# Performance work log

Measured on AMD Instinct MI355X. Metric: run time of the kernel, lower is better.

The kernel has to match this reference:

```python
import jax, jax.numpy as jnp
import numpy as np

NUM_USERS = 100000
NUM_ITEMS = 50000
EMB_DIM = 64
NNZ = 4800000
BATCH = 16384
N_LAYERS = 3


def setup_inputs() -> dict:
    key = jax.random.key(0)
    k0, k1, k2, k3, k4, k5 = jax.random.split(key, 6)
    N = NUM_USERS + NUM_ITEMS
    rows = jax.random.randint(k0, (NNZ,), 0, N, dtype=jnp.int32)
    cols = jax.random.randint(k1, (NNZ,), 0, N, dtype=jnp.int32)
    # symmetric normalization values: 1/sqrt(deg_out * deg_in), as in LightGCN preprocessing
    ones = jnp.ones((NNZ,), jnp.float32)
    deg_r = jax.ops.segment_sum(ones, rows, num_segments=N)
    deg_c = jax.ops.segment_sum(ones, cols, num_segments=N)
    vals = 1.0 / jnp.sqrt(jnp.maximum(deg_r[rows], 1.0) * jnp.maximum(deg_c[cols], 1.0))
    user_emb = 0.1 * jax.random.normal(k2, (NUM_USERS, EMB_DIM), jnp.float32)
    item_emb = 0.1 * jax.random.normal(k3, (NUM_ITEMS, EMB_DIM), jnp.float32)
    user_idx = jax.random.randint(k4, (BATCH,), 0, NUM_USERS, dtype=jnp.int64)
    item_idx = jax.random.randint(k5, (BATCH,), 0, NUM_ITEMS, dtype=jnp.int64)
    return {
        "user_emb": user_emb,
        "item_emb": item_emb,
        "rows": rows,
        "cols": cols,
        "vals": vals,
        "user_idx": user_idx,
        "item_idx": item_idx,
        "n_layers": N_LAYERS,
    }


def reference(user_emb, item_emb, rows, cols, vals, user_idx, item_idx, n_layers):
    num_users = user_emb.shape[0]
    N = num_users + item_emb.shape[0]
    all_emb = jnp.concatenate([user_emb, item_emb], axis=0)  # [N, D]
    acc = all_emb  # running sum over layer embeddings (embs[0] = E)
    emb = all_emb
    for _ in range(n_layers):
        # SpMM: out[r] = sum_{edges (r,c)} vals * emb[c]
        emb = jax.ops.segment_sum(vals[:, None] * emb[cols], rows, num_segments=N)
        acc = acc + emb
    light_out = acc / jnp.float32(n_layers + 1)  # mean over stacked layers
    u_e = light_out[user_idx]                     # [B, D]
    i_e = light_out[num_users + item_idx]         # [B, D]
    return (u_e * i_e).sum(axis=-1)               # [B]
```

## Files before the change

### kernel.cpp

```cpp
#include <hip/hip_runtime.h>
#include <hip/hip_fp16.h>

#define NUM_USERS 100000
#define NUM_ITEMS 50000
#define NN (NUM_USERS + NUM_ITEMS)
#define EMB_DIM 64
#define BATCH 16384
#define RPA 512
#define NBA ((NN + RPA - 1) / RPA)
#define SLOT 22528
#define NBLKA 768
#define CAP 16
#define OVF 32
#define SENT (1 << 27)
#define RSLOT 72

__device__ __forceinline__ unsigned h2u(__half2 h) {
    union { __half2 h; unsigned u; } x; x.h = h; return x.u;
}
__device__ __forceinline__ __half2 u2h(unsigned u) {
    union { __half2 h; unsigned u; } x; x.u = u; return x.h;
}

__global__ void lgcn_prep(unsigned long long* __restrict__ gq,
                          unsigned char* __restrict__ flags) {
    int i = blockIdx.x * blockDim.x + threadIdx.x;
    if (i < NBA) gq[i] = 0;
    for (int j = i; j < NN / 4; j += gridDim.x * blockDim.x)
        ((unsigned*)flags)[j] = 0;
    if (i == 0)
        for (int j = (NN / 4) * 4; j < NN; ++j) flags[j] = 0;
}

__global__ void __launch_bounds__(512) lgcn_binA(
        const float4* __restrict__ user_emb, const float4* __restrict__ item_emb,
        uint2* __restrict__ embh, int n_user4, int n_tot4,
        const int* __restrict__ rows, const int* __restrict__ cols,
        const float* __restrict__ vals, unsigned long long* __restrict__ gq,
        int2* __restrict__ cv_tmp, int nnz, int epb) {
    __shared__ int2 stage[CAP][NBA];
    __shared__ int  hist[NBA];
    __shared__ int  SBase[NBA];
    __shared__ int  pcnt[NBA];
    __shared__ int4 ovfBuf[2][OVF];
    __shared__ int  ovfCnt[2];
    int t = threadIdx.x;

    for (int i = blockIdx.x * 512 + t; i < n_tot4; i += NBLKA * 512) {
        float4 v = (i < n_user4) ? user_emb[i] : item_emb[i - n_user4];
        uint2 o;
        o.x = h2u(__float22half2_rn(make_float2(v.x, v.y)));
        o.y = h2u(__float22half2_rn(make_float2(v.z, v.w)));
        embh[i] = o;
    }

    int base = blockIdx.x * epb;
    int end  = base + epb; if (end > nnz) end = nnz;
    if (t < NBA) { hist[t] = 0; pcnt[t] = 0; }
    if (t == 0) { ovfCnt[0] = 0; ovfCnt[1] = 0; }
    __syncthreads();
    for (int i = base + t; i < end; i += 512)
        atomicAdd(&hist[rows[i] >> 9], 1);
    __syncthreads();
    if (t < NBA) {
        int c = hist[t];
        int p = 0;
        if (c) {
            int cp = (c + 7) & ~7;
            unsigned long long old = atomicAdd(&gq[t],
                ((unsigned long long)c << 32) | (unsigned)cp);
            p = (int)(unsigned)old;
        }
        SBase[t] = p;
    }
    __syncthreads();

    int p = 0;
    for (int r0 = base; r0 < end; r0 += 1024, p ^= 1) {
        int no = ovfCnt[p ^ 1];
        for (int j = t; j < no; j += 512) {
            int4 e = ovfBuf[p ^ 1][j];
            int b = e.w;
            int k = atomicAdd(&pcnt[b], 1);
            if (k < CAP) stage[k][b] = make_int2(e.x, e.y);
            else { int q = atomicAdd(&ovfCnt[p], 1);
                   if (q < OVF) ovfBuf[p][q] = e; }
        }
#pragma unroll
        for (int q2 = 0; q2 < 2; ++q2) {
            int i = r0 + q2 * 512 + t;
            if (i < end) {
                int r = rows[i];
                int b = r >> 9;
                __half hv = __float2half(vals[i]);
                int ex = ((r & 511) << 18) | cols[i];
                int ey = (int)h2u(__half2half2(hv));
                int k = atomicAdd(&pcnt[b], 1);
                if (k < CAP) stage[k][b] = make_int2(ex, ey);
                else { int q = atomicAdd(&ovfCnt[p], 1);
                       if (q < OVF) ovfBuf[p][q] = make_int4(ex, ey, 0, b); }
            }
        }
        __syncthreads();
        if (t < NBA) {
            int c = pcnt[t]; if (c > CAP) c = CAP;
            int g = c & ~7;
            if (g) {
                long long gb = (long long)t * SLOT + SBase[t];
                int4* dst = (int4*)&cv_tmp[gb];
                for (int j = 0; j < g; j += 2) {
                    int2 e0 = stage[j][t];
                    int2 e1 = stage[j + 1][t];
                    dst[j >> 1] = make_int4(e0.x, e0.y, e1.x, e1.y);
                }
                SBase[t] += g;
                for (int j = g; j < c; ++j) stage[j - g][t] = stage[j][t];
            }
            pcnt[t] = c - g;
        }
        if (t == 0) ovfCnt[p ^ 1] = 0;
        __syncthreads();
    }

    {
        int no = ovfCnt[p ^ 1];
        for (int j = t; j < no; j += 512) {
            int4 e = ovfBuf[p ^ 1][j];
            int b = e.w;
            int k = atomicAdd(&pcnt[b], 1);
            if (k < CAP) stage[k][b] = make_int2(e.x, e.y);
            else cv_tmp[(long long)b * SLOT + SBase[b] + k] =
                     make_int2(e.x, e.y);
        }
    }
    __syncthreads();
    if (t < NBA) {
        int c_raw = pcnt[t];
        int cl = min(c_raw, CAP);
        long long gb = (long long)t * SLOT + SBase[t];
        for (int j = 0; j < cl; ++j) cv_tmp[gb + j] = stage[j][t];
        int cp = (c_raw + 7) & ~7;
        for (int j = c_raw; j < cp; ++j) cv_tmp[gb + j] = make_int2(SENT, 0);
    }
}

#define BINB_PUT(p) do { int x = (p).x; if (!(x & SENT)) {                   \
    int rl = (x >> 18) & 511; int pos = atomicAdd(&cnt[rl], 1);              \
    if (pos < RSLOT) { int v16 = (p).y & 0xFFFF;                             \
        cv[(long long)(r0 + rl) * RSLOT + pos] =                             \
            (((v16 + 2) >> 2) << 18) | (x & 0x3FFFF); } } } while (0)

__global__ void __launch_bounds__(1024) lgcn_binB(
        const unsigned long long* __restrict__ gq,
        const int2* __restrict__ cv_tmp, int* __restrict__ cv,
        int* __restrict__ deg,
        const int* __restrict__ user_idx, const int* __restrict__ item_idx,
        unsigned char* __restrict__ flags) {
    __shared__ int cnt[RPA];
    int s = blockIdx.x;
    int t = threadIdx.x;
    long long w0 = (long long)s * SLOT;
    int wlen = (int)(unsigned)gq[s];
    int r0 = s * RPA;
    if (t < RPA) cnt[t] = 0;
    __syncthreads();
    int i = t;
    for (; i + 3 * 1024 < wlen; i += 4096) {
        int2 p0 = cv_tmp[w0 + i];
        int2 p1 = cv_tmp[w0 + i + 1024];
        int2 p2 = cv_tmp[w0 + i + 2048];
        int2 p3 = cv_tmp[w0 + i + 3072];
        BINB_PUT(p0); BINB_PUT(p1); BINB_PUT(p2); BINB_PUT(p3);
    }
    for (; i < wlen; i += 1024) {
        int2 p = cv_tmp[w0 + i];
        BINB_PUT(p);
    }
    for (int j = s * 1024 + t; j < BATCH; j += NBA * 1024) {
        flags[user_idx[j]] = 1;
        flags[NUM_USERS + item_idx[j]] = 1;
    }
    __syncthreads();
    if (t < RPA) {
        int r = r0 + t;
        if (r < NN) deg[r] = min(cnt[t], RSLOT);
    }
}

__global__ void __launch_bounds__(256) lgcn_spmm(
        const int* __restrict__ deg,
        const int* __restrict__ cv,
        const uint4* __restrict__ embh,
        uint4* __restrict__ nxth,
        const unsigned char* __restrict__ flags, int sel,
        const uint4* __restrict__ e0t, const uint4* __restrict__ e1t,
        float4* __restrict__ sums) {
    int wid = (blockIdx.x * blockDim.x + threadIdx.x) >> 6;
    int lane = threadIdx.x & 63;
    if (wid >= NN) return;
    if (sel && !flags[wid]) return;
    int n = deg[wid];
    int grp  = lane >> 3;
    int dim8 = lane & 7;
    const int* ep = cv + (long long)wid * RSLOT;

    __half2 c0 = __float2half2_rn(0.f);
    __half2 c1 = c0, c2 = c0, c3 = c0;
    int m = n >> 3;
    int k = 0;
    for (; k + 4 <= m; k += 4) {
        int p[4]; uint4 raw[4];
#pragma unroll
        for (int j = 0; j < 4; ++j) p[j] = ep[8 * (k + j) + grp];
#pragma unroll
        for (int j = 0; j < 4; ++j)
            raw[j] = embh[(long long)(p[j] & 0x3FFFF) * 8 + dim8];
#pragma unroll
        for (int j = 0; j < 4; ++j) {
            unsigned vv = ((unsigned)p[j] >> 18) << 2;
            __half2 v2 = u2h(vv | (vv << 16));
            c0 = __hfma2(v2, u2h(raw[j].x), c0);
            c1 = __hfma2(v2, u2h(raw[j].y), c1);
            c2 = __hfma2(v2, u2h(raw[j].z), c2);
            c3 = __hfma2(v2, u2h(raw[j].w), c3);
        }
    }
    for (; k + 2 <= m; k += 2) {
        int p[2]; uint4 raw[2];
#pragma unroll
        for (int j = 0; j < 2; ++j) p[j] = ep[8 * (k + j) + grp];
#pragma unroll
        for (int j = 0; j < 2; ++j)
            raw[j] = embh[(long long)(p[j] & 0x3FFFF) * 8 + dim8];
#pragma unroll
        for (int j = 0; j < 2; ++j) {
            unsigned vv = ((unsigned)p[j] >> 18) << 2;
            __half2 v2 = u2h(vv | (vv << 16));
            c0 = __hfma2(v2, u2h(raw[j].x), c0);
            c1 = __hfma2(v2, u2h(raw[j].y), c1);
            c2 = __hfma2(v2, u2h(raw[j].z), c2);
            c3 = __hfma2(v2, u2h(raw[j].w), c3);
        }
    }
    for (; k < m; ++k) {
        int p = ep[8 * k + grp];
        uint4 raw = embh[(long long)(p & 0x3FFFF) * 8 + dim8];
        unsigned vv = ((unsigned)p >> 18) << 2;
        __half2 v2 = u2h(vv | (vv << 16));
        c0 = __hfma2(v2, u2h(raw.x), c0);
        c1 = __hfma2(v2, u2h(raw.y), c1);
        c2 = __hfma2(v2, u2h(raw.z), c2);
        c3 = __hfma2(v2, u2h(raw.w), c3);
    }
    int rem = n & 7;
    if (grp < rem) {
        int p = ep[8 * m + grp];
        uint4 raw = embh[(long long)(p & 0x3FFFF) * 8 + dim8];
        unsigned vv = ((unsigned)p >> 18) << 2;
        __half2 v2 = u2h(vv | (vv << 16));
        c0 = __hfma2(v2, u2h(raw.x), c0);
        c1 = __hfma2(v2, u2h(raw.y), c1);
        c2 = __hfma2(v2, u2h(raw.z), c2);
        c3 = __hfma2(v2, u2h(raw.w), c3);
    }

#pragma unroll
    for (int off = 8; off < 64; off <<= 1) {
        c0 = __hadd2(c0, u2h(__shfl_xor(h2u(c0), off)));
        c1 = __hadd2(c1, u2h(__shfl_xor(h2u(c1), off)));
        c2 = __hadd2(c2, u2h(__shfl_xor(h2u(c2), off)));
        c3 = __hadd2(c3, u2h(__shfl_xor(h2u(c3), off)));
    }
    if (grp == 0) {
        long long o = (long long)wid * 8 + dim8;
        if (!sel) {
            uint4 ov;
            ov.x = h2u(c0); ov.y = h2u(c1); ov.z = h2u(c2); ov.w = h2u(c3);
            nxth[o] = ov;
        } else {
            uint4 r0v = e0t[o], r1v = e1t[o], r2v = embh[o];
            float2 f0 = __half22float2(c0), f1 = __half22float2(c1);
            float2 f2 = __half22float2(c2), f3 = __half22float2(c3);
            float2 a;
            a = __half22float2(u2h(r0v.x)); f0.x += a.x; f0.y += a.y;
            a = __half22float2(u2h(r1v.x)); f0.x += a.x; f0.y += a.y;
            a = __half22float2(u2h(r2v.x)); f0.x += a.x; f0.y += a.y;
            a = __half22float2(u2h(r0v.y)); f1.x += a.x; f1.y += a.y;
            a = __half22float2(u2h(r1v.y)); f1.x += a.x; f1.y += a.y;
            a = __half22float2(u2h(r2v.y)); f1.x += a.x; f1.y += a.y;
            a = __half22float2(u2h(r0v.z)); f2.x += a.x; f2.y += a.y;
            a = __half22float2(u2h(r1v.z)); f2.x += a.x; f2.y += a.y;
            a = __half22float2(u2h(r2v.z)); f2.x += a.x; f2.y += a.y;
            a = __half22float2(u2h(r0v.w)); f3.x += a.x; f3.y += a.y;
            a = __half22float2(u2h(r1v.w)); f3.x += a.x; f3.y += a.y;
            a = __half22float2(u2h(r2v.w)); f3.x += a.x; f3.y += a.y;
            long long so = (long long)wid * 16 + dim8 * 2;
            sums[so]     = make_float4(f0.x, f0.y, f1.x, f1.y);
            sums[so + 1] = make_float4(f2.x, f2.y, f3.x, f3.y);
        }
    }
}

__global__ void lgcn_dot(const float4* __restrict__ sums,
                         const int* __restrict__ user_idx,
                         const int* __restrict__ item_idx,
                         float* __restrict__ out, int batch) {
    int t = blockIdx.x * blockDim.x + threadIdx.x;
    int b = t >> 4;
    if (b >= batch) return;
    int l = t & 15;
    float4 su = sums[(long long)user_idx[b] * 16 + l];
    float4 si = sums[(long long)(NUM_USERS + item_idx[b]) * 16 + l];
    float s = su.x * si.x + su.y * si.y + su.z * si.z + su.w * si.w;
    s += __shfl_down(s, 8, 16);
    s += __shfl_down(s, 4, 16);
    s += __shfl_down(s, 2, 16);
    s += __shfl_down(s, 1, 16);
    if (l == 0) out[b] = s * (1.0f / 16.0f);
}

extern "C" void kernel_launch(void* const* d_in, const int* in_sizes, int n_in,
                              void* d_out, int out_size, void* d_ws, size_t ws_size,
                              hipStream_t stream) {
    const float* user_emb = (const float*)d_in[0];
    const float* item_emb = (const float*)d_in[1];
    const int*   rows     = (const int*)d_in[2];
    const int*   cols     = (const int*)d_in[3];
    const float* vals     = (const float*)d_in[4];
    const int*   user_idx = (const int*)d_in[5];
    const int*   item_idx = (const int*)d_in[6];
    float* out = (float*)d_out;

    const int nnz = in_sizes[2];
    const size_t node_uint2 = (size_t)NN * 16;

    uint2* E[4];
    E[0] = (uint2*)d_ws;
    E[1] = E[0] + node_uint2;
    E[2] = E[1] + node_uint2;
    E[3] = E[2] + node_uint2;
    int*    cv   = (int*)(E[3] + node_uint2);
    float4* sums = (float4*)(cv + (size_t)NN * RSLOT);
    int*    deg  = (int*)(sums + (size_t)NN * 16);
    unsigned long long* gq = (unsigned long long*)(deg + NN);
    unsigned char* flags = (unsigned char*)(gq + NBA);
    int2*   cv_tmp = (int2*)E[1];

    const int n_tot4  = NN * EMB_DIM / 4;
    const int n_user4 = NUM_USERS * EMB_DIM / 4;
    const int epb = (nnz + NBLKA - 1) / NBLKA;

    lgcn_prep<<<64, 256, 0, stream>>>(gq, flags);

    lgcn_binA<<<NBLKA, 512, 0, stream>>>(
        (const float4*)user_emb, (const float4*)item_emb, E[0],
        n_user4, n_tot4, rows, cols, vals, gq, cv_tmp, nnz, epb);

    lgcn_binB<<<NBA, 1024, 0, stream>>>(gq, cv_tmp, cv, deg,
                                        user_idx, item_idx, flags);

    const int spmm_blocks = (NN * 64 + 255) / 256;
    for (int layer = 0; layer < 3; ++layer) {
        lgcn_spmm<<<spmm_blocks, 256, 0, stream>>>(deg, cv,
                                                   (const uint4*)E[layer],
                                                   (uint4*)E[layer + 1],
                                                   flags, layer == 2 ? 1 : 0,
                                                   (const uint4*)E[0],
                                                   (const uint4*)E[1], sums);
    }

    lgcn_dot<<<(BATCH * 16 + 255) / 256, 256, 0, stream>>>(
        sums, user_idx, item_idx, out, BATCH);
}
```

Baseline: 413.7 us.

## Rewrite edge binning as block-local counting sort and split second pass four ways

The first binning kernel now uses a shared-memory counting sort. Each block histograms its edges, gives every row-bucket a contiguous region of a shared edge buffer, scatters edges there, and then writes each bucket out with coalesced wave-wide stores. This replaces the small CAP staging ring and its overflow buffers, and the block count goes from 768 to 1024. The second binning pass now runs four 256-thread blocks per 512-row bucket, each taking a quarter of the bucket's edges. Each block counts its own edges, reserves per-row offsets with global atomics on deg (now zeroed in prep), and the SpMM clamps deg to RSLOT. The aims are to raise parallelism and cut serialized staging and flush loops, at the cost of an extra counting pass and global atomics; EPB is hardcoded, so nnz/NBLKA must not exceed it.

```diff
diff --git a/kernel.cpp b/kernel.cpp
--- a/kernel.cpp
+++ b/kernel.cpp
@@ -9,9 +9,9 @@
 #define RPA 512
 #define NBA ((NN + RPA - 1) / RPA)
 #define SLOT 22528
-#define NBLKA 768
-#define CAP 16
-#define OVF 32
+#define NBLKA 1024
+#define EPB 4688
+#define NBB (NBA * 4)
 #define SENT (1 << 27)
 #define RSLOT 72
 
@@ -23,13 +23,13 @@
 }
 
 __global__ void lgcn_prep(unsigned long long* __restrict__ gq,
+                          int* __restrict__ deg,
                           unsigned char* __restrict__ flags) {
     int i = blockIdx.x * blockDim.x + threadIdx.x;
+    int g = gridDim.x * blockDim.x;
     if (i < NBA) gq[i] = 0;
-    for (int j = i; j < NN / 4; j += gridDim.x * blockDim.x)
-        ((unsigned*)flags)[j] = 0;
-    if (i == 0)
-        for (int j = (NN / 4) * 4; j < NN; ++j) flags[j] = 0;
+    for (int j = i; j < NN; j += g) deg[j] = 0;
+    for (int j = i; j < NN / 4; j += g) ((unsigned*)flags)[j] = 0;
 }
 
 __global__ void __launch_bounds__(512) lgcn_binA(
@@ -38,12 +38,12 @@
         const int* __restrict__ rows, const int* __restrict__ cols,
         const float* __restrict__ vals, unsigned long long* __restrict__ gq,
         int2* __restrict__ cv_tmp, int nnz, int epb) {
-    __shared__ int2 stage[CAP][NBA];
+    __shared__ int2 edges[EPB];
     __shared__ int  hist[NBA];
-    __shared__ int  SBase[NBA];
-    __shared__ int  pcnt[NBA];
-    __shared__ int4 ovfBuf[2][OVF];
-    __shared__ int  ovfCnt[2];
+    __shared__ int  lofs[NBA];
+    __shared__ int  lcur[NBA];
+    __shared__ int  gbase[NBA];
+    __shared__ int  ltot;
     int t = threadIdx.x;
 
     for (int i = blockIdx.x * 512 + t; i < n_tot4; i += NBLKA * 512) {
@@ -56,134 +56,96 @@
 
     int base = blockIdx.x * epb;
     int end  = base + epb; if (end > nnz) end = nnz;
-    if (t < NBA) { hist[t] = 0; pcnt[t] = 0; }
-    if (t == 0) { ovfCnt[0] = 0; ovfCnt[1] = 0; }
+    if (t < NBA) { hist[t] = 0; lcur[t] = 0; }
+    if (t == 0) ltot = 0;
     __syncthreads();
     for (int i = base + t; i < end; i += 512)
         atomicAdd(&hist[rows[i] >> 9], 1);
     __syncthreads();
     if (t < NBA) {
         int c = hist[t];
-        int p = 0;
         if (c) {
+            lofs[t] = atomicAdd(&ltot, c);
             int cp = (c + 7) & ~7;
             unsigned long long old = atomicAdd(&gq[t],
                 ((unsigned long long)c << 32) | (unsigned)cp);
-            p = (int)(unsigned)old;
+            gbase[t] = (int)(unsigned)old;
         }
-        SBase[t] = p;
-    }
-    __syncthreads();
-
-    int p = 0;
-    for (int r0 = base; r0 < end; r0 += 1024, p ^= 1) {
-        int no = ovfCnt[p ^ 1];
-        for (int j = t; j < no; j += 512) {
-            int4 e = ovfBuf[p ^ 1][j];
-            int b = e.w;
-            int k = atomicAdd(&pcnt[b], 1);
-            if (k < CAP) stage[k][b] = make_int2(e.x, e.y);
-            else { int q = atomicAdd(&ovfCnt[p], 1);
-                   if (q < OVF) ovfBuf[p][q] = e; }
-        }
-#pragma unroll
-        for (int q2 = 0; q2 < 2; ++q2) {
-            int i = r0 + q2 * 512 + t;
-            if (i < end) {
-                int r = rows[i];
-                int b = r >> 9;
-                __half hv = __float2half(vals[i]);
-                int ex = ((r & 511) << 18) | cols[i];
-                int ey = (int)h2u(__half2half2(hv));
-                int k = atomicAdd(&pcnt[b], 1);
-                if (k < CAP) stage[k][b] = make_int2(ex, ey);
-                else { int q = atomicAdd(&ovfCnt[p], 1);
-                       if (q < OVF) ovfBuf[p][q] = make_int4(ex, ey, 0, b); }
-            }
-        }
-        __syncthreads();
-        if (t < NBA) {
-            int c = pcnt[t]; if (c > CAP) c = CAP;
-            int g = c & ~7;
-            if (g) {
-                long long gb = (long long)t * SLOT + SBase[t];
-                int4* dst = (int4*)&cv_tmp[gb];
-                for (int j = 0; j < g; j += 2) {
-                    int2 e0 = stage[j][t];
-                    int2 e1 = stage[j + 1][t];
-                    dst[j >> 1] = make_int4(e0.x, e0.y, e1.x, e1.y);
-                }
-                SBase[t] += g;
-                for (int j = g; j < c; ++j) stage[j - g][t] = stage[j][t];
-            }
-            pcnt[t] = c - g;
-        }
-        if (t == 0) ovfCnt[p ^ 1] = 0;
-        __syncthreads();
-    }
-
-    {
-        int no = ovfCnt[p ^ 1];
-        for (int j = t; j < no; j += 512) {
-            int4 e = ovfBuf[p ^ 1][j];
-            int b = e.w;
-            int k = atomicAdd(&pcnt[b], 1);
-            if (k < CAP) stage[k][b] = make_int2(e.x, e.y);
-            else cv_tmp[(long long)b * SLOT + SBase[b] + k] =
-                     make_int2(e.x, e.y);
-        }
-    }
-    __syncthreads();
-    if (t < NBA) {
-        int c_raw = pcnt[t];
-        int cl = min(c_raw, CAP);
-        long long gb = (long long)t * SLOT + SBase[t];
-        for (int j = 0; j < cl; ++j) cv_tmp[gb + j] = stage[j][t];
-        int cp = (c_raw + 7) & ~7;
-        for (int j = c_raw; j < cp; ++j) cv_tmp[gb + j] = make_int2(SENT, 0);
-    }
-}
-
-#define BINB_PUT(p) do { int x = (p).x; if (!(x & SENT)) {                   \
-    int rl = (x >> 18) & 511; int pos = atomicAdd(&cnt[rl], 1);              \
+    }
+    __syncthreads();
+    for (int i = base + t; i < end; i += 512) {
+        int r = rows[i];
+        int b = r >> 9;
+        int k = atomicAdd(&lcur[b], 1);
+        __half hv = __float2half(vals[i]);
+        edges[lofs[b] + k] = make_int2(((r & 511) << 18) | cols[i],
+                                       (int)h2u(__half2half2(hv)));
+    }
+    __syncthreads();
+    int w = t >> 6, lane = t & 63;
+    for (int b = w; b < NBA; b += 8) {
+        int c = hist[b];
+        if (!c) continue;
+        int cp = (c + 7) & ~7;
+        long long dst = (long long)b * SLOT + gbase[b];
+        int lo = lofs[b];
+        for (int j = lane; j < cp; j += 64)
+            cv_tmp[dst + j] = (j < c) ? edges[lo + j] : make_int2(SENT, 0);
+    }
+}
+
+#define BPUT(p) do { int x = (p).x; if (!(x & SENT)) {                       \
+    int rl = (x >> 18) & 511;                                                \
+    int pos = bse[rl] + atomicAdd(&lcnt[rl], 1);                             \
     if (pos < RSLOT) { int v16 = (p).y & 0xFFFF;                             \
         cv[(long long)(r0 + rl) * RSLOT + pos] =                             \
             (((v16 + 2) >> 2) << 18) | (x & 0x3FFFF); } } } while (0)
 
-__global__ void __launch_bounds__(1024) lgcn_binB(
+__global__ void __launch_bounds__(256) lgcn_binB(
         const unsigned long long* __restrict__ gq,
         const int2* __restrict__ cv_tmp, int* __restrict__ cv,
         int* __restrict__ deg,
         const int* __restrict__ user_idx, const int* __restrict__ item_idx,
         unsigned char* __restrict__ flags) {
     __shared__ int cnt[RPA];
-    int s = blockIdx.x;
+    __shared__ int bse[RPA];
+    __shared__ int lcnt[RPA];
+    int s = blockIdx.x >> 2;
+    int q = blockIdx.x & 3;
     int t = threadIdx.x;
     long long w0 = (long long)s * SLOT;
     int wlen = (int)(unsigned)gq[s];
+    int qs = (int)(((long long)wlen * q) >> 2);
+    int qe = (int)(((long long)wlen * (q + 1)) >> 2);
     int r0 = s * RPA;
-    if (t < RPA) cnt[t] = 0;
-    __syncthreads();
-    int i = t;
-    for (; i + 3 * 1024 < wlen; i += 4096) {
+    for (int j = t; j < RPA; j += 256) cnt[j] = 0;
+    __syncthreads();
+    for (int i = qs + t; i < qe; i += 256) {
+        int x = cv_tmp[w0 + i].x;
+        if (!(x & SENT)) atomicAdd(&cnt[(x >> 18) & 511], 1);
+    }
+    __syncthreads();
+    for (int j = t; j < RPA; j += 256) {
+        int c = cnt[j];
+        if (c) bse[j] = atomicAdd(&deg[r0 + j], c);
+        lcnt[j] = 0;
+    }
+    __syncthreads();
+    int i = qs + t;
+    for (; i + 3 * 256 < qe; i += 1024) {
         int2 p0 = cv_tmp[w0 + i];
-        int2 p1 = cv_tmp[w0 + i + 1024];
-        int2 p2 = cv_tmp[w0 + i + 2048];
-        int2 p3 = cv_tmp[w0 + i + 3072];
-        BINB_PUT(p0); BINB_PUT(p1); BINB_PUT(p2); BINB_PUT(p3);
-    }
-    for (; i < wlen; i += 1024) {
+        int2 p1 = cv_tmp[w0 + i + 256];
+        int2 p2 = cv_tmp[w0 + i + 512];
+        int2 p3 = cv_tmp[w0 + i + 768];
+        BPUT(p0); BPUT(p1); BPUT(p2); BPUT(p3);
+    }
+    for (; i < qe; i += 256) {
         int2 p = cv_tmp[w0 + i];
-        BINB_PUT(p);
-    }
-    for (int j = s * 1024 + t; j < BATCH; j += NBA * 1024) {
+        BPUT(p);
+    }
+    for (int j = blockIdx.x * 256 + t; j < BATCH; j += NBB * 256) {
         flags[user_idx[j]] = 1;
         flags[NUM_USERS + item_idx[j]] = 1;
-    }
-    __syncthreads();
-    if (t < RPA) {
-        int r = r0 + t;
-        if (r < NN) deg[r] = min(cnt[t], RSLOT);
     }
 }
 
@@ -200,6 +162,7 @@
     if (wid >= NN) return;
     if (sel && !flags[wid]) return;
     int n = deg[wid];
+    if (n > RSLOT) n = RSLOT;
     int grp  = lane >> 3;
     int dim8 = lane & 7;
     const int* ep = cv + (long long)wid * RSLOT;
@@ -350,14 +313,14 @@
     const int n_user4 = NUM_USERS * EMB_DIM / 4;
     const int epb = (nnz + NBLKA - 1) / NBLKA;
 
-    lgcn_prep<<<64, 256, 0, stream>>>(gq, flags);
+    lgcn_prep<<<128, 256, 0, stream>>>(gq, deg, flags);
 
     lgcn_binA<<<NBLKA, 512, 0, stream>>>(
         (const float4*)user_emb, (const float4*)item_emb, E[0],
         n_user4, n_tot4, rows, cols, vals, gq, cv_tmp, nnz, epb);
 
-    lgcn_binB<<<NBA, 1024, 0, stream>>>(gq, cv_tmp, cv, deg,
-                                        user_idx, item_idx, flags);
+    lgcn_binB<<<NBB, 256, 0, stream>>>(gq, cv_tmp, cv, deg,
+                                       user_idx, item_idx, flags);
 
     const int spmm_blocks = (NN * 64 + 255) / 256;
     for (int layer = 0; layer < 3; ++layer) {
```

New measurement: 444.7 us. +7.5%, slower.
